# Performance work log

Hardware: AMD Instinct MI355X
Metric: run time of the kernel (lower is better)

Reference implementation:

```python
import jax, jax.numpy as jnp
import numpy as np

B, D, O = 16384, 1024, 1024
NUM_TASKS = 2
E = 4  # experts per group (2 task groups + 1 shared group)


def setup_inputs() -> dict:
    key = jax.random.key(0)
    ks = jax.random.split(key, 7)
    x = jax.random.normal(ks[0], (B, D), dtype=jnp.float32)
    # Stacked expert params: groups g in {task0, task1, shared}, each with E experts.
    W = jax.random.normal(ks[1], (3, E, D, O), dtype=jnp.float32) * 0.02  # Linear weight (in,out layout)
    b = jax.random.normal(ks[2], (3, E, O), dtype=jnp.float32) * 0.02
    # Per-task gates over (E specific + E shared) = 8 experts.
    Wg = jax.random.normal(ks[3], (NUM_TASKS, D, 2 * E), dtype=jnp.float32) * 0.02
    bg = jax.random.normal(ks[4], (NUM_TASKS, 2 * E), dtype=jnp.float32) * 0.02
    # Shared gate over all 3*E = 12 experts (is_top=False).
    Wgs = jax.random.normal(ks[5], (D, 3 * E), dtype=jnp.float32) * 0.02
    bgs = jax.random.normal(ks[6], (3 * E,), dtype=jnp.float32) * 0.02
    return {"x": x, "W": W, "b": b, "Wg": Wg, "bg": bg, "Wgs": Wgs, "bgs": bgs}


def reference(x, W, b, Wg, bg, Wgs, bgs):
    # All 12 experts share the same input (single-input branch): one batched GEMM.
    # h: [3, B, E, O]  (dropout is identity in eval mode)
    h = jax.nn.relu(jnp.einsum('bd,gedo->gbeo', x, W) + b[:, None, :, :])
    # Per-task gates: [T, B, 2E]
    sel_t = jax.nn.softmax(jnp.einsum('bd,tdm->tbm', x, Wg) + bg[:, None, :], axis=-1)
    outs = []
    for t in range(NUM_TASKS):
        mat = jnp.concatenate([h[t], h[2]], axis=1)  # [B, 2E, O]
        outs.append(jnp.einsum('bmo,bm->bo', mat, sel_t[t]))
    # Shared gate over all experts (is_top=False): [B, 3E]
    sel_s = jax.nn.softmax(x @ Wgs + bgs, axis=-1)
    mat_all = jnp.concatenate([h[0], h[1], h[2]], axis=1)  # [B, 3E, O]
    outs.append(jnp.einsum('bmo,bm->bo', mat_all, sel_s))
    return tuple(outs)
```

## Files before the change

### kernel.cpp

```cpp
#include <hip/hip_runtime.h>

typedef unsigned short ushort_t;
typedef __attribute__((ext_vector_type(8))) short short8;
typedef __attribute__((ext_vector_type(4))) float floatx4;

#define B_ROWS 16384
#define BO 16777216
#define MC 4096

__device__ __forceinline__ ushort_t f2bf(float f){
  unsigned u = __float_as_uint(f);
  u += 0x7fffu + ((u >> 16) & 1u);
  return (ushort_t)(u >> 16);
}
__device__ __forceinline__ float bf2f(ushort_t u){
  return __uint_as_float(((unsigned)u) << 16);
}

__device__ __forceinline__ void gld_lds16(void* l, const void* g){
  __builtin_amdgcn_global_load_lds(
      (__attribute__((address_space(1))) void*)(g),
      (__attribute__((address_space(3))) void*)(l), 16, 0, 0);
}

__global__ void cvt_x(const float* __restrict__ x, ushort_t* __restrict__ xb){
  const int i = (blockIdx.x * 256 + threadIdx.x) * 4;
  const floatx4 v = *(const floatx4*)(x + i);
  ushort4 o;
  o.x = f2bf(v[0]); o.y = f2bf(v[1]); o.z = f2bf(v[2]); o.w = f2bf(v[3]);
  *(ushort4*)(xb + i) = o;
}

__global__ void cvt_wt(const float* __restrict__ W, ushort_t* __restrict__ wt){
  __shared__ float t[64][65];
  const int blk = blockIdx.x;
  const int ge = blk >> 8, dt = (blk >> 4) & 15, ot = blk & 15;
  const float* src = W + ((size_t)ge << 20) + (size_t)(dt * 64) * 1024 + ot * 64;
  const int c4 = (threadIdx.x & 15) * 4, r0 = threadIdx.x >> 4;
#pragma unroll
  for (int p = 0; p < 4; ++p){
    const int r = r0 + p * 16;
    const floatx4 v = *(const floatx4*)(src + (size_t)r * 1024 + c4);
    t[r][c4] = v[0]; t[r][c4+1] = v[1]; t[r][c4+2] = v[2]; t[r][c4+3] = v[3];
  }
  __syncthreads();
  ushort_t* dst = wt + ((size_t)ge << 20) + (size_t)(ot * 64) * 1024 + dt * 64;
  const int d4 = (threadIdx.x & 15) * 4, o0 = threadIdx.x >> 4;
#pragma unroll
  for (int p = 0; p < 4; ++p){
    const int o = o0 + p * 16;
    ushort4 ov;
    ov.x = f2bf(t[d4][o]);   ov.y = f2bf(t[d4+1][o]);
    ov.z = f2bf(t[d4+2][o]); ov.w = f2bf(t[d4+3][o]);
    *(ushort4*)(dst + (size_t)o * 1024 + d4) = ov;
  }
}

__global__ void cvt_wg(const float* __restrict__ Wg, const float* __restrict__ bg,
                       const float* __restrict__ Wgs, const float* __restrict__ bgs,
                       ushort_t* __restrict__ wgcat, float* __restrict__ biascat){
  const int m = blockIdx.x;
#pragma unroll
  for (int j = 0; j < 4; ++j){
    const int d = j * 256 + threadIdx.x;
    float v;
    if (m < 16)      v = Wg[((size_t)((m >> 3) * 1024 + d)) * 8 + (m & 7)];
    else if (m < 28) v = Wgs[(size_t)d * 12 + (m - 16)];
    else             v = 0.f;
    wgcat[m * 1024 + d] = f2bf(v);
  }
  if (threadIdx.x == 0){
    float bv;
    if (m < 16)      bv = bg[m];
    else if (m < 28) bv = bgs[m - 16];
    else             bv = -1e30f;
    biascat[m] = bv;
  }
}

__global__ __launch_bounds__(256) void gates_mfma(
    const ushort_t* __restrict__ xb, const ushort_t* __restrict__ wgcat,
    const float* __restrict__ biascat, float* __restrict__ selT)
{
  __shared__ __align__(16) char gsm[20480];
  const int tid = threadIdx.x;
  const int lane = tid & 63;
  const int w = tid >> 6;
  const int lr = lane & 15;
  const int brow = blockIdx.x * 128;

  const int sc = (((tid & 7) ^ ((tid >> 3) & 7)) << 4);
  const char* aS = (const char*)xb + (size_t)(brow + (tid >> 3)) * 2048 + sc;
  const char* bS = (const char*)wgcat + (size_t)(tid >> 3) * 2048 + sc;

  const int kx0 = (((lane >> 4) << 4)) ^ ((lane & 7) << 4);
  const int kx1 = (64 + ((lane >> 4) << 4)) ^ ((lane & 7) << 4);

  int aOff[2], bOff[2];
#pragma unroll
  for (int m = 0; m < 2; ++m) aOff[m] = (w * 32 + m * 16 + lr) * 128;
#pragma unroll
  for (int n = 0; n < 2; ++n) bOff[n] = 16384 + (n * 16 + lr) * 128;

  const floatx4 fz = {0.f, 0.f, 0.f, 0.f};
  floatx4 hacc[2][2];
#pragma unroll
  for (int m = 0; m < 2; ++m)
#pragma unroll
    for (int n = 0; n < 2; ++n) hacc[m][n] = fz;

  for (int kt = 0; kt < 16; ++kt){
    const size_t ko = (size_t)kt * 128;
#pragma unroll
    for (int j = 0; j < 4; ++j)
      gld_lds16(gsm + j * 4096 + w * 1024, aS + (size_t)j * 65536 + ko);
    gld_lds16(gsm + 16384 + w * 1024, bS + ko);
    __syncthreads();
    short8 av[2][2], bv[2][2];
#pragma unroll
    for (int m = 0; m < 2; ++m){
      av[m][0] = *(const short8*)(gsm + aOff[m] + kx0);
      av[m][1] = *(const short8*)(gsm + aOff[m] + kx1);
    }
#pragma unroll
    for (int n = 0; n < 2; ++n){
      bv[n][0] = *(const short8*)(gsm + bOff[n] + kx0);
      bv[n][1] = *(const short8*)(gsm + bOff[n] + kx1);
    }
#pragma unroll
    for (int m = 0; m < 2; ++m)
#pragma unroll
      for (int n = 0; n < 2; ++n){
        hacc[m][n] = __builtin_amdgcn_mfma_f32_16x16x32_bf16(av[m][0], bv[n][0], hacc[m][n], 0, 0, 0);
        hacc[m][n] = __builtin_amdgcn_mfma_f32_16x16x32_bf16(av[m][1], bv[n][1], hacc[m][n], 0, 0, 0);
      }
    __syncthreads();
  }

  const float bc0 = biascat[lr];
  const float bc1 = biascat[16 + lr];
#pragma unroll
  for (int m = 0; m < 2; ++m){
#pragma unroll
    for (int r = 0; r < 4; ++r){
      float l0 = hacc[m][0][r] + bc0;
      float l1 = hacc[m][1][r] + bc1;
      float mx0 = l0;
#pragma unroll
      for (int s = 1; s < 8; s <<= 1) mx0 = fmaxf(mx0, __shfl_xor(mx0, s, 64));
      float e0 = __expf(l0 - mx0);
      float s0 = e0;
#pragma unroll
      for (int s = 1; s < 8; s <<= 1) s0 += __shfl_xor(s0, s, 64);
      float mx1 = l1;
#pragma unroll
      for (int s = 1; s < 16; s <<= 1) mx1 = fmaxf(mx1, __shfl_xor(mx1, s, 64));
      float e1 = __expf(l1 - mx1);
      float s1 = e1;
#pragma unroll
      for (int s = 1; s < 16; s <<= 1) s1 += __shfl_xor(s1, s, 64);
      const int row = brow + w * 32 + m * 16 + ((lane >> 4) << 2) + r;
      selT[(size_t)lr * B_ROWS + row] = e0 / s0;
      if (lr < 12) selT[(size_t)(16 + lr) * B_ROWS + row] = e1 / s1;
    }
  }
}

__global__ __launch_bounds__(512, 2) void pass1_gemm(
    const ushort_t* __restrict__ xb,
    const ushort_t* __restrict__ wt,
    const float* __restrict__ bias,
    ushort_t* __restrict__ h,
    int chunk_row0)
{
  __shared__ __align__(16) char smem[131072];
  const int tid  = threadIdx.x;
  const int lane = tid & 63;
  const int wv   = tid >> 6;
  const int wm   = wv >> 2;
  const int wn   = wv & 3;
  const int lr   = lane & 15;
  const int NT   = 48;

  const int bid = blockIdx.x;
  const int L = (bid & 7) * 32 + (bid >> 3);
  const int eg = L >> 6;
  const int nt = (L >> 4) & 3;
  const int mt = L & 15;
  const int brow_l = mt * 256;
  const int browg  = chunk_row0 + brow_l;
  const int bcol   = nt * 256;

  const int sc = (((tid & 7) ^ ((tid >> 3) & 7)) << 4);
  const char* aSrc[2];
  size_t bOffBase[2];
#pragma unroll
  for (int hh = 0; hh < 2; ++hh){
    aSrc[hh] = (const char*)xb + (size_t)(browg + hh * 128 + (tid >> 3)) * 2048 + sc;
    bOffBase[hh] = (size_t)(bcol + hh * 128 + (tid >> 3)) * 2048 + sc;
  }

  auto stageA = [&](int hh, int kt, int bo){
    char* d = smem + bo + hh * 16384 + wv * 1024;
    const char* s = aSrc[hh] + (size_t)(kt & 15) * 128;
    gld_lds16(d, s);
    gld_lds16(d + 8192, s + 131072);
  };
  auto stageB = [&](int hh, int kt, int bo){
    const int exk = eg * 3 + (kt >> 4);
    char* d = smem + bo + 32768 + hh * 16384 + wv * 1024;
    const char* s = (const char*)wt + ((size_t)exk << 21) + bOffBase[hh]
                  + (size_t)(kt & 15) * 128;
    gld_lds16(d, s);
    gld_lds16(d + 8192, s + 131072);
  };

  const int kx0 = (((lane >> 4) << 4)) ^ ((lane & 7) << 4);
  const int kx1 = (64 + ((lane >> 4) << 4)) ^ ((lane & 7) << 4);
  int aOff[8], bOff[4];
#pragma unroll
  for (int m = 0; m < 8; ++m) aOff[m] = wm * 16384 + (m * 16 + lr) * 128;
#pragma unroll
  for (int n = 0; n < 4; ++n)
    bOff[n] = 32768 + (wn >> 1) * 16384 + ((wn & 1) * 64 + n * 16 + lr) * 128;

  const floatx4 fz = {0.f, 0.f, 0.f, 0.f};
  floatx4 hacc[8][4];
#pragma unroll
  for (int m = 0; m < 8; ++m)
#pragma unroll
    for (int n = 0; n < 4; ++n) hacc[m][n] = fz;

  const int colw = bcol + wn * 64;
  const int g4 = (lane >> 4) << 2;
  auto EPI = [&](int el){
    const int exk = eg * 3 + el;
    ushort_t* hbase = h + ((size_t)exk * MC) * 1024;
    floatx4 bv[4];
#pragma unroll
    for (int n = 0; n < 4; ++n)
      bv[n] = *(const floatx4*)(bias + exk * 1024 + colw + n * 16 + g4);
#pragma unroll
    for (int m = 0; m < 8; ++m){
      const int row = brow_l + wm * 128 + m * 16 + lr;
      ushort_t* hp = hbase + (size_t)row * 1024 + colw + g4;
#pragma unroll
      for (int n = 0; n < 4; ++n){
        const float v0 = fmaxf(hacc[m][n][0] + bv[n][0], 0.f);
        const float v1 = fmaxf(hacc[m][n][1] + bv[n][1], 0.f);
        const float v2 = fmaxf(hacc[m][n][2] + bv[n][2], 0.f);
        const float v3 = fmaxf(hacc[m][n][3] + bv[n][3], 0.f);
        uint2 pk;
        pk.x = (unsigned)f2bf(v0) | ((unsigned)f2bf(v1) << 16);
        pk.y = (unsigned)f2bf(v2) | ((unsigned)f2bf(v3) << 16);
        *(uint2*)(hp + n * 16) = pk;
        hacc[m][n] = fz;
      }
    }
  };

#define LDF(X) (*(const short8*)(smem + (X)))
#define MFMA_(A, Bv, C) __builtin_amdgcn_mfma_f32_16x16x32_bf16(A, Bv, C, 0, 0, 0)

  stageA(0, 0, 0); stageA(1, 0, 0); stageB(0, 0, 0); stageB(1, 0, 0);
  stageB(0, 1, 65536);
  asm volatile("s_waitcnt vmcnt(2)" ::: "memory");
  __builtin_amdgcn_s_barrier();
  __builtin_amdgcn_sched_barrier(0);

  short8 a0[4][2], b0[2][2], b1[2][2];
#pragma unroll
  for (int m = 0; m < 4; ++m){
    a0[m][0] = LDF(aOff[m] + kx0);
    a0[m][1] = LDF(aOff[m] + kx1);
  }
#pragma unroll
  for (int n = 0; n < 2; ++n){
    b0[n][0] = LDF(bOff[n] + kx0);
    b0[n][1] = LDF(bOff[n] + kx1);
    b1[n][0] = LDF(bOff[2 + n] + kx0);
    b1[n][1] = LDF(bOff[2 + n] + kx1);
  }

  for (int i = 0; i < NT; ++i){
    const int cur = (i & 1) << 16;
    const int nxt = cur ^ 65536;

    short8 a1[4][2];
#pragma unroll
    for (int m = 0; m < 4; ++m){
      a1[m][0] = LDF(cur + aOff[4 + m] + kx0);
      a1[m][1] = LDF(cur + aOff[4 + m] + kx1);
    }
    if (i + 1 < NT){ stageA(0, i + 1, nxt); stageA(1, i + 1, nxt); stageB(1, i + 1, nxt); }
    __builtin_amdgcn_sched_barrier(0);
    __builtin_amdgcn_s_setprio(1);
#pragma unroll
    for (int m = 0; m < 4; ++m)
#pragma unroll
      for (int n = 0; n < 2; ++n){
        hacc[m][n]     = MFMA_(b0[n][0], a0[m][0], hacc[m][n]);
        hacc[m][n]     = MFMA_(b0[n][1], a0[m][1], hacc[m][n]);
        hacc[m][2 + n] = MFMA_(b1[n][0], a0[m][0], hacc[m][2 + n]);
        hacc[m][2 + n] = MFMA_(b1[n][1], a0[m][1], hacc[m][2 + n]);
      }
    __builtin_amdgcn_s_setprio(0);
    __builtin_amdgcn_s_barrier();

    if (i + 2 < NT) stageB(0, i + 2, cur);
    __builtin_amdgcn_sched_barrier(0);
    __builtin_amdgcn_s_setprio(1);
#pragma unroll
    for (int m = 0; m < 4; ++m)
#pragma unroll
      for (int n = 0; n < 2; ++n){
        hacc[4 + m][n]     = MFMA_(b0[n][0], a1[m][0], hacc[4 + m][n]);
        hacc[4 + m][n]     = MFMA_(b0[n][1], a1[m][1], hacc[4 + m][n]);
        hacc[4 + m][2 + n] = MFMA_(b1[n][0], a1[m][0], hacc[4 + m][2 + n]);
        hacc[4 + m][2 + n] = MFMA_(b1[n][1], a1[m][1], hacc[4 + m][2 + n]);
      }
    __builtin_amdgcn_s_setprio(0);
    if ((i & 15) == 15) EPI(i >> 4);

    if (i < NT - 2){
      if ((i & 15) == 15) { asm volatile("s_waitcnt vmcnt(34)" ::: "memory"); }
      else                { asm volatile("s_waitcnt vmcnt(2)"  ::: "memory"); }
    } else if (i == NT - 2){
      asm volatile("s_waitcnt vmcnt(0)" ::: "memory");
    }
    if (i + 1 < NT){
      __builtin_amdgcn_s_barrier();
      __builtin_amdgcn_sched_barrier(0);
#pragma unroll
      for (int m = 0; m < 4; ++m){
        a0[m][0] = LDF(nxt + aOff[m] + kx0);
        a0[m][1] = LDF(nxt + aOff[m] + kx1);
      }
#pragma unroll
      for (int n = 0; n < 2; ++n){
        b0[n][0] = LDF(nxt + bOff[n] + kx0);
        b0[n][1] = LDF(nxt + bOff[n] + kx1);
        b1[n][0] = LDF(nxt + bOff[2 + n] + kx0);
        b1[n][1] = LDF(nxt + bOff[2 + n] + kx1);
      }
    }
  }
#undef LDF
#undef MFMA_
}

__global__ __launch_bounds__(256) void combine_kernel(
    const ushort_t* __restrict__ h,
    const float* __restrict__ selT,
    float* __restrict__ out,
    int row0)
{
  const int tid = threadIdx.x;
  const int lb  = blockIdx.x * 2 + (tid >> 7);
  const int b   = row0 + lb;
  const int c   = (tid & 127) * 8;
  const ushort_t* hp = h + (size_t)lb * 1024 + c;

  float a0[8], a1[8], as_[8];
#pragma unroll
  for (int k = 0; k < 8; ++k){ a0[k] = 0.f; a1[k] = 0.f; as_[k] = 0.f; }

#pragma unroll
  for (int e = 0; e < 4; ++e){
    const float w0 = selT[(size_t)e * B_ROWS + b];
    const float ws = selT[(size_t)(16 + e) * B_ROWS + b];
    const short8 hv = *(const short8*)(hp + (size_t)e * (MC * 1024));
#pragma unroll
    for (int k = 0; k < 8; ++k){
      const float f = bf2f((ushort_t)hv[k]);
      a0[k] += w0 * f; as_[k] += ws * f;
    }
  }
#pragma unroll
  for (int e = 0; e < 4; ++e){
    const float w1 = selT[(size_t)(8 + e) * B_ROWS + b];
    const float ws = selT[(size_t)(20 + e) * B_ROWS + b];
    const short8 hv = *(const short8*)(hp + (size_t)(4 + e) * (MC * 1024));
#pragma unroll
    for (int k = 0; k < 8; ++k){
      const float f = bf2f((ushort_t)hv[k]);
      a1[k] += w1 * f; as_[k] += ws * f;
    }
  }
#pragma unroll
  for (int e = 0; e < 4; ++e){
    const float w0 = selT[(size_t)(4 + e) * B_ROWS + b];
    const float w1 = selT[(size_t)(12 + e) * B_ROWS + b];
    const float ws = selT[(size_t)(24 + e) * B_ROWS + b];
    const short8 hv = *(const short8*)(hp + (size_t)(8 + e) * (MC * 1024));
#pragma unroll
    for (int k = 0; k < 8; ++k){
      const float f = bf2f((ushort_t)hv[k]);
      a0[k] += w0 * f; a1[k] += w1 * f; as_[k] += ws * f;
    }
  }

  float* o0 = out + (size_t)b * 1024 + c;
  *(floatx4*)(o0)     = *(const floatx4*)(a0);
  *(floatx4*)(o0 + 4) = *(const floatx4*)(a0 + 4);
  float* o1 = o0 + BO;
  *(floatx4*)(o1)     = *(const floatx4*)(a1);
  *(floatx4*)(o1 + 4) = *(const floatx4*)(a1 + 4);
  float* o2 = o1 + BO;
  *(floatx4*)(o2)     = *(const floatx4*)(as_);
  *(floatx4*)(o2 + 4) = *(const floatx4*)(as_ + 4);
}

__global__ void gates_kernel(const float* __restrict__ x,
                             const float* __restrict__ Wg,
                             const float* __restrict__ bg,
                             const float* __restrict__ Wgs,
                             const float* __restrict__ bgs,
                             float* __restrict__ selT)
{
  const int lane = threadIdx.x & 63;
  const int w    = threadIdx.x >> 6;
  const int b    = blockIdx.x * 4 + w;
  const float* xr = x + (size_t)b * 1024;
  float acc[28];
#pragma unroll
  for (int m = 0; m < 28; ++m) acc[m] = 0.f;
#pragma unroll
  for (int j = 0; j < 4; ++j){
    const int d0 = (j * 64 + lane) * 4;
    const floatx4 xv = *(const floatx4*)(xr + d0);
#pragma unroll
    for (int q = 0; q < 4; ++q){
      const float xs = xv[q];
      const int d = d0 + q;
      const float* g0 = Wg + d * 8;
      const float* g1 = Wg + 8192 + d * 8;
      const float* gs = Wgs + d * 12;
#pragma unroll
      for (int m = 0; m < 8; ++m)  acc[m]      += xs * g0[m];
#pragma unroll
      for (int m = 0; m < 8; ++m)  acc[8 + m]  += xs * g1[m];
#pragma unroll
      for (int m = 0; m < 12; ++m) acc[16 + m] += xs * gs[m];
    }
  }
#pragma unroll
  for (int m = 0; m < 28; ++m){
    float v = acc[m];
#pragma unroll
    for (int off = 1; off < 64; off <<= 1) v += __shfl_xor(v, off, 64);
    acc[m] = v;
  }
  if (lane == 0){
    float e0[8], e1[8], es[12];
    float mx0 = -1e30f, mx1 = -1e30f, mxs = -1e30f;
#pragma unroll
    for (int m = 0; m < 8; ++m){  e0[m] = acc[m]      + bg[m];     mx0 = fmaxf(mx0, e0[m]); }
#pragma unroll
    for (int m = 0; m < 8; ++m){  e1[m] = acc[8 + m]  + bg[8 + m]; mx1 = fmaxf(mx1, e1[m]); }
#pragma unroll
    for (int m = 0; m < 12; ++m){ es[m] = acc[16 + m] + bgs[m];    mxs = fmaxf(mxs, es[m]); }
    float s0 = 0.f, s1 = 0.f, ss = 0.f;
#pragma unroll
    for (int m = 0; m < 8; ++m){  e0[m] = __expf(e0[m] - mx0); s0 += e0[m]; }
#pragma unroll
    for (int m = 0; m < 8; ++m){  e1[m] = __expf(e1[m] - mx1); s1 += e1[m]; }
#pragma unroll
    for (int m = 0; m < 12; ++m){ es[m] = __expf(es[m] - mxs); ss += es[m]; }
    const float r0 = 1.f / s0, r1 = 1.f / s1, rs = 1.f / ss;
#pragma unroll
    for (int m = 0; m < 8; ++m)  selT[(size_t)m * B_ROWS + b]        = e0[m] * r0;
#pragma unroll
    for (int m = 0; m < 8; ++m)  selT[(size_t)(8 + m) * B_ROWS + b]  = e1[m] * r1;
#pragma unroll
    for (int m = 0; m < 12; ++m) selT[(size_t)(16 + m) * B_ROWS + b] = es[m] * rs;
  }
}

__global__ __launch_bounds__(256, 2) void moe_kernel(
    const ushort_t* __restrict__ xb,
    const ushort_t* __restrict__ wt,
    const float* __restrict__ bias,
    const float* __restrict__ selT,
    float* __restrict__ out)
{
  __shared__ __align__(16) char smem[24576];
  const int tid  = threadIdx.x;
  const int lane = tid & 63;
  const int wid  = tid >> 6;
  const int wm   = wid >> 1;
  const int wn   = wid & 1;
  const int brow = (blockIdx.x >> 4) << 7;
  const int bcol = (blockIdx.x & 15) << 6;
  const int rstg = tid >> 3;
  const int scol = ((tid & 7) << 4) ^ ((rstg & 7) << 4);
  size_t aoff[4], boff[2];
#pragma unroll
  for (int i = 0; i < 4; ++i) aoff[i] = (size_t)(brow + i * 32 + rstg) * 2048 + scol;
#pragma unroll
  for (int i = 0; i < 2; ++i) boff[i] = (size_t)(bcol + i * 32 + rstg) * 2048 + scol;
  char* aldst = smem + wid * 1024;
  char* bldst = smem + 16384 + wid * 1024;
  const int kl   = (lane >> 4) << 4;
  const int swzr = (lane & 7) << 4;
  int arow[4], brw[2];
#pragma unroll
  for (int m = 0; m < 4; ++m) arow[m] = (wm * 64 + m * 16 + (lane & 15)) * 128;
#pragma unroll
  for (int n = 0; n < 2; ++n) brw[n] = 16384 + (wn * 32 + n * 16 + (lane & 15)) * 128;
  const floatx4 fz = {0.f, 0.f, 0.f, 0.f};
  floatx4 o0a[4][2], o1a[4][2], osa[4][2];
#pragma unroll
  for (int m = 0; m < 4; ++m)
#pragma unroll
    for (int n = 0; n < 2; ++n){ o0a[m][n] = fz; o1a[m][n] = fz; osa[m][n] = fz; }
  const int c0 = bcol + wn * 32 + (lane & 15);
  const int rb = brow + wm * 64 + ((lane >> 4) << 2);
  for (int ex = 0; ex < 12; ++ex){
    floatx4 hacc[4][2];
#pragma unroll
    for (int m = 0; m < 4; ++m)
#pragma unroll
      for (int n = 0; n < 2; ++n) hacc[m][n] = fz;
    const size_t wbase = (size_t)ex << 21;
    for (int kt = 0; kt < 16; ++kt){
      const size_t ko = (size_t)kt << 7;
#pragma unroll
      for (int i = 0; i < 4; ++i)
        gld_lds16(aldst + i * 4096, (const char*)xb + aoff[i] + ko);
#pragma unroll
      for (int i = 0; i < 2; ++i)
        gld_lds16(bldst + i * 4096, (const char*)wt + wbase + boff[i] + ko);
      __syncthreads();
#pragma unroll
      for (int kk = 0; kk < 2; ++kk){
        short8 av[4], bv[2];
        const int kb = (kk << 6) + kl;
#pragma unroll
        for (int m = 0; m < 4; ++m)
          av[m] = *(const short8*)(smem + arow[m] + (kb ^ swzr));
#pragma unroll
        for (int n = 0; n < 2; ++n)
          bv[n] = *(const short8*)(smem + brw[n] + (kb ^ swzr));
#pragma unroll
        for (int m = 0; m < 4; ++m)
#pragma unroll
          for (int n = 0; n < 2; ++n)
            hacc[m][n] = __builtin_amdgcn_mfma_f32_16x16x32_bf16(av[m], bv[n], hacc[m][n], 0, 0, 0);
      }
      __syncthreads();
    }
    const int g = ex >> 2, e = ex & 3;
    const float bi0 = bias[ex * 1024 + c0];
    const float bi1 = bias[ex * 1024 + c0 + 16];
    int i0, i1, is_;
    if (g == 0)      { i0 = e;     i1 = -1;     is_ = 16 + e; }
    else if (g == 1) { i0 = -1;    i1 = 8 + e;  is_ = 20 + e; }
    else             { i0 = 4 + e; i1 = 12 + e; is_ = 24 + e; }
#pragma unroll
    for (int m = 0; m < 4; ++m){
      const int rg = rb + m * 16;
      const floatx4 wsv = *(const floatx4*)(selT + (size_t)is_ * B_ROWS + rg);
      floatx4 w0 = fz, w1 = fz;
      if (i0 >= 0) w0 = *(const floatx4*)(selT + (size_t)i0 * B_ROWS + rg);
      if (i1 >= 0) w1 = *(const floatx4*)(selT + (size_t)i1 * B_ROWS + rg);
#pragma unroll
      for (int n = 0; n < 2; ++n){
        const float bi = n ? bi1 : bi0;
#pragma unroll
        for (int r = 0; r < 4; ++r){
          float hv = hacc[m][n][r] + bi;
          hv = fmaxf(hv, 0.f);
          osa[m][n][r] += wsv[r] * hv;
          o0a[m][n][r] += w0[r] * hv;
          o1a[m][n][r] += w1[r] * hv;
        }
      }
    }
  }
#pragma unroll
  for (int m = 0; m < 4; ++m){
#pragma unroll
    for (int n = 0; n < 2; ++n){
#pragma unroll
      for (int r = 0; r < 4; ++r){
        const size_t idx = (size_t)(rb + m * 16 + r) * 1024 + (c0 + (n << 4));
        out[idx]          = o0a[m][n][r];
        out[idx + BO]     = o1a[m][n][r];
        out[idx + 2 * BO] = osa[m][n][r];
      }
    }
  }
}

extern "C" void kernel_launch(void* const* d_in, const int* in_sizes, int n_in,
                              void* d_out, int out_size, void* d_ws, size_t ws_size,
                              hipStream_t stream) {
  const float* x   = (const float*)d_in[0];
  const float* W   = (const float*)d_in[1];
  const float* b   = (const float*)d_in[2];
  const float* Wg  = (const float*)d_in[3];
  const float* bg  = (const float*)d_in[4];
  const float* Wgs = (const float*)d_in[5];
  const float* bgs = (const float*)d_in[6];
  float* out = (float*)d_out;

  char* ws = (char*)d_ws;
  ushort_t* xb   = (ushort_t*)ws;
  ushort_t* wtp  = (ushort_t*)(ws + 33554432);
  float*    selT = (float*)(ws + 58720256);
  ushort_t* wgc  = (ushort_t*)(ws + 60555264);
  float*    bcat = (float*)(ws + 60620800);
  ushort_t* hbuf = (ushort_t*)(ws + 67108864);

  const bool two_pass = ws_size >= (size_t)(67108864 + 12 * MC * 1024 * 2);

  cvt_x<<<dim3(16384), dim3(256), 0, stream>>>(x, xb);
  cvt_wt<<<dim3(3072), dim3(256), 0, stream>>>(W, wtp);

  if (two_pass){
    cvt_wg<<<dim3(32), dim3(256), 0, stream>>>(Wg, bg, Wgs, bgs, wgc, bcat);
    gates_mfma<<<dim3(128), dim3(256), 0, stream>>>(xb, wgc, bcat, selT);
    for (int c = 0; c < 16384 / MC; ++c){
      pass1_gemm<<<dim3(256), dim3(512), 0, stream>>>(xb, wtp, b, hbuf, c * MC);
      combine_kernel<<<dim3(MC / 2), dim3(256), 0, stream>>>(hbuf, selT, out, c * MC);
    }
  } else {
    gates_kernel<<<dim3(4096), dim3(256), 0, stream>>>(x, Wg, bg, Wgs, bgs, selT);
    moe_kernel<<<dim3(2048), dim3(256), 0, stream>>>(xb, wtp, b, selT, out);
  }
}
```

Measured before the change: 683.2 us.

## Restructure GEMM main loop to prefetch two K-tiles ahead with one barrier

Rewrites the software pipeline of the expert GEMM main loop. Global-to-LDS staging now runs two tiles ahead, with all four stages issued after a single mid-iteration barrier, instead of being split across two barriers. B fragments for the next tile are ping-ponged in registers via a manually unrolled-by-two loop, and A fragments are read from LDS at the start of each iteration. The aim is to cut barriers per iteration and hide global latency better. In exchange it holds more in-flight loads and uses more registers for the double B fragments, and the vmcnt waits change, including a full vmcnt(0) drain in most iterations.

```diff
diff --git a/kernel.cpp b/kernel.cpp
--- a/kernel.cpp
+++ b/kernel.cpp
@@ -263,87 +263,88 @@
 #define MFMA_(A, Bv, C) __builtin_amdgcn_mfma_f32_16x16x32_bf16(A, Bv, C, 0, 0, 0)
 
   stageA(0, 0, 0); stageA(1, 0, 0); stageB(0, 0, 0); stageB(1, 0, 0);
-  stageB(0, 1, 65536);
-  asm volatile("s_waitcnt vmcnt(2)" ::: "memory");
+  stageA(0, 1, 65536); stageA(1, 1, 65536); stageB(0, 1, 65536); stageB(1, 1, 65536);
+  asm volatile("s_waitcnt vmcnt(8)" ::: "memory");
   __builtin_amdgcn_s_barrier();
   __builtin_amdgcn_sched_barrier(0);
 
-  short8 a0[4][2], b0[2][2], b1[2][2];
-#pragma unroll
-  for (int m = 0; m < 4; ++m){
-    a0[m][0] = LDF(aOff[m] + kx0);
-    a0[m][1] = LDF(aOff[m] + kx1);
-  }
+  short8 b0A[2][2], b1A[2][2], b0B[2][2], b1B[2][2];
 #pragma unroll
   for (int n = 0; n < 2; ++n){
-    b0[n][0] = LDF(bOff[n] + kx0);
-    b0[n][1] = LDF(bOff[n] + kx1);
-    b1[n][0] = LDF(bOff[2 + n] + kx0);
-    b1[n][1] = LDF(bOff[2 + n] + kx1);
-  }
-
-  for (int i = 0; i < NT; ++i){
+    b0A[n][0] = LDF(bOff[n] + kx0);
+    b0A[n][1] = LDF(bOff[n] + kx1);
+    b1A[n][0] = LDF(bOff[2 + n] + kx0);
+    b1A[n][1] = LDF(bOff[2 + n] + kx1);
+  }
+
+  auto ITER = [&](int i, short8 (&B0C)[2][2], short8 (&B1C)[2][2],
+                         short8 (&B0N)[2][2], short8 (&B1N)[2][2]){
     const int cur = (i & 1) << 16;
     const int nxt = cur ^ 65536;
 
-    short8 a1[4][2];
+    short8 a0[4][2], a1[4][2];
+#pragma unroll
+    for (int m = 0; m < 4; ++m){
+      a0[m][0] = LDF(cur + aOff[m] + kx0);
+      a0[m][1] = LDF(cur + aOff[m] + kx1);
+    }
 #pragma unroll
     for (int m = 0; m < 4; ++m){
       a1[m][0] = LDF(cur + aOff[4 + m] + kx0);
       a1[m][1] = LDF(cur + aOff[4 + m] + kx1);
     }
-    if (i + 1 < NT){ stageA(0, i + 1, nxt); stageA(1, i + 1, nxt); stageB(1, i + 1, nxt); }
     __builtin_amdgcn_sched_barrier(0);
     __builtin_amdgcn_s_setprio(1);
 #pragma unroll
     for (int m = 0; m < 4; ++m)
 #pragma unroll
       for (int n = 0; n < 2; ++n){
-        hacc[m][n]     = MFMA_(b0[n][0], a0[m][0], hacc[m][n]);
-        hacc[m][n]     = MFMA_(b0[n][1], a0[m][1], hacc[m][n]);
-        hacc[m][2 + n] = MFMA_(b1[n][0], a0[m][0], hacc[m][2 + n]);
-        hacc[m][2 + n] = MFMA_(b1[n][1], a0[m][1], hacc[m][2 + n]);
+        hacc[m][n]     = MFMA_(B0C[n][0], a0[m][0], hacc[m][n]);
+        hacc[m][n]     = MFMA_(B0C[n][1], a0[m][1], hacc[m][n]);
+        hacc[m][2 + n] = MFMA_(B1C[n][0], a0[m][0], hacc[m][2 + n]);
+        hacc[m][2 + n] = MFMA_(B1C[n][1], a0[m][1], hacc[m][2 + n]);
       }
     __builtin_amdgcn_s_setprio(0);
-    __builtin_amdgcn_s_barrier();
-
-    if (i + 2 < NT) stageB(0, i + 2, cur);
+
+    if (i < NT - 1){
+      asm volatile("s_waitcnt lgkmcnt(0)" ::: "memory");
+      if (i == 16 || i == 32) { asm volatile("s_waitcnt vmcnt(32)" ::: "memory"); }
+      else                    { asm volatile("s_waitcnt vmcnt(0)"  ::: "memory"); }
+      __builtin_amdgcn_s_barrier();
+      __builtin_amdgcn_sched_barrier(0);
+    }
+
+    if (i + 1 < NT){
+#pragma unroll
+      for (int n = 0; n < 2; ++n){
+        B0N[n][0] = LDF(nxt + bOff[n] + kx0);
+        B0N[n][1] = LDF(nxt + bOff[n] + kx1);
+        B1N[n][0] = LDF(nxt + bOff[2 + n] + kx0);
+        B1N[n][1] = LDF(nxt + bOff[2 + n] + kx1);
+      }
+    }
+    if (i + 2 < NT){
+      stageA(0, i + 2, cur); stageA(1, i + 2, cur);
+      stageB(0, i + 2, cur); stageB(1, i + 2, cur);
+    }
     __builtin_amdgcn_sched_barrier(0);
     __builtin_amdgcn_s_setprio(1);
 #pragma unroll
     for (int m = 0; m < 4; ++m)
 #pragma unroll
       for (int n = 0; n < 2; ++n){
-        hacc[4 + m][n]     = MFMA_(b0[n][0], a1[m][0], hacc[4 + m][n]);
-        hacc[4 + m][n]     = MFMA_(b0[n][1], a1[m][1], hacc[4 + m][n]);
-        hacc[4 + m][2 + n] = MFMA_(b1[n][0], a1[m][0], hacc[4 + m][2 + n]);
-        hacc[4 + m][2 + n] = MFMA_(b1[n][1], a1[m][1], hacc[4 + m][2 + n]);
+        hacc[4 + m][n]     = MFMA_(B0C[n][0], a1[m][0], hacc[4 + m][n]);
+        hacc[4 + m][n]     = MFMA_(B0C[n][1], a1[m][1], hacc[4 + m][n]);
+        hacc[4 + m][2 + n] = MFMA_(B1C[n][0], a1[m][0], hacc[4 + m][2 + n]);
+        hacc[4 + m][2 + n] = MFMA_(B1C[n][1], a1[m][1], hacc[4 + m][2 + n]);
       }
     __builtin_amdgcn_s_setprio(0);
     if ((i & 15) == 15) EPI(i >> 4);
-
-    if (i < NT - 2){
-      if ((i & 15) == 15) { asm volatile("s_waitcnt vmcnt(34)" ::: "memory"); }
-      else                { asm volatile("s_waitcnt vmcnt(2)"  ::: "memory"); }
-    } else if (i == NT - 2){
-      asm volatile("s_waitcnt vmcnt(0)" ::: "memory");
-    }
-    if (i + 1 < NT){
-      __builtin_amdgcn_s_barrier();
-      __builtin_amdgcn_sched_barrier(0);
-#pragma unroll
-      for (int m = 0; m < 4; ++m){
-        a0[m][0] = LDF(nxt + aOff[m] + kx0);
-        a0[m][1] = LDF(nxt + aOff[m] + kx1);
-      }
-#pragma unroll
-      for (int n = 0; n < 2; ++n){
-        b0[n][0] = LDF(nxt + bOff[n] + kx0);
-        b0[n][1] = LDF(nxt + bOff[n] + kx1);
-        b1[n][0] = LDF(nxt + bOff[2 + n] + kx0);
-        b1[n][1] = LDF(nxt + bOff[2 + n] + kx1);
-      }
-    }
+  };
+
+  for (int ii = 0; ii < NT; ii += 2){
+    ITER(ii,     b0A, b1A, b0B, b1B);
+    ITER(ii + 1, b0B, b1B, b0A, b1A);
   }
 #undef LDF
 #undef MFMA_
```

Result: slower. 1.338 ms (+95.9%).
